# Kernel optimization log

Hardware: AMD Instinct MI355X
Metric: run time of the kernel (lower is better)

Reference implementation:

```python
import jax, jax.numpy as jnp
import numpy as np

B, S, D_IN, D_OUT = 4, 4096, 2048, 2048


def setup_inputs() -> dict:
    key = jax.random.key(0)
    kx, kw = jax.random.split(key)
    x = jax.random.normal(kx, (B, S, D_IN), dtype=jnp.float32)
    weight = jax.random.normal(kw, (D_OUT, D_IN), dtype=jnp.float32) * 0.02
    return {"x": x, "weight": weight}


def reference(x, weight):
    # Per-row absmax int8 activation quantization
    x_scale = jnp.clip(jnp.max(jnp.abs(x), axis=-1, keepdims=True), 1e-05, None)  # [B,S,1]
    x_quant = jnp.clip(jnp.round(x / x_scale * 127.0), -128.0, 127.0)
    # Ternary weight quantization (mean-centered absmean scale)
    w_mean = jnp.mean(weight)
    w_centered = weight - w_mean
    w_scale = jnp.clip(jnp.mean(jnp.abs(w_centered)), 1e-05, None)
    w_quant = jnp.clip(jnp.round(w_centered / w_scale), -1.0, 1.0)
    # GEMM on quantized values, then dequant rescale
    y = jnp.einsum('bsi,oi->bso', x_quant, w_quant)  # [B,S,D_OUT]
    y = y * (w_scale * x_scale / 127.0)
    return y.astype(x.dtype)
```

## Files before the change

kernel.cpp:

```cpp
#include <hip/hip_runtime.h>
#include <stdint.h>

#define M_TOT 16384
#define K_DIM 2048
#define N_DIM 2048
#define W_ELEMS (N_DIM * K_DIM)

typedef int v4i __attribute__((ext_vector_type(4)));

__device__ __forceinline__ void async_load16(const void* gptr, void* lptr) {
    __builtin_amdgcn_global_load_lds(
        (__attribute__((address_space(1))) void*)(uintptr_t)gptr,
        (__attribute__((address_space(3))) void*)(uint32_t)(uintptr_t)lptr,
        16, 0, 0);
}

__device__ __forceinline__ int qclamp(float v, int lo, int hi) {
    int q = (int)rintf(v);
    q = q > hi ? hi : (q < lo ? lo : q);
    return q & 255;
}

__global__ __launch_bounds__(256) void wsum_kernel(const float* __restrict__ w,
                                                   double* __restrict__ spart) {
    int tid = blockIdx.x * 256 + threadIdx.x;
    const float4* w4 = (const float4*)w;
    double s = 0.0;
    #pragma unroll
    for (int it = 0; it < 8; it++) {
        float4 v = w4[tid + it * 131072];
        s += (double)v.x + (double)v.y + (double)v.z + (double)v.w;
    }
    #pragma unroll
    for (int off = 32; off; off >>= 1) s += __shfl_down(s, off);
    __shared__ double ls[4];
    if ((threadIdx.x & 63) == 0) ls[threadIdx.x >> 6] = s;
    __syncthreads();
    if (threadIdx.x == 0) spart[blockIdx.x] = ls[0] + ls[1] + ls[2] + ls[3];
}

__global__ __launch_bounds__(256) void wabs_kernel(const float* __restrict__ w,
                                                   const double* __restrict__ spart,
                                                   double* __restrict__ apart) {
    __shared__ double ls[4];
    double sm = spart[threadIdx.x] + spart[threadIdx.x + 256];
    #pragma unroll
    for (int off = 32; off; off >>= 1) sm += __shfl_down(sm, off);
    if ((threadIdx.x & 63) == 0) ls[threadIdx.x >> 6] = sm;
    __syncthreads();
    double mean = (ls[0] + ls[1] + ls[2] + ls[3]) * (1.0 / (double)W_ELEMS);
    __syncthreads();
    int tid = blockIdx.x * 256 + threadIdx.x;
    const float4* w4 = (const float4*)w;
    double s = 0.0;
    #pragma unroll
    for (int it = 0; it < 8; it++) {
        float4 v = w4[tid + it * 131072];
        s += fabs((double)v.x - mean) + fabs((double)v.y - mean) +
             fabs((double)v.z - mean) + fabs((double)v.w - mean);
    }
    #pragma unroll
    for (int off = 32; off; off >>= 1) s += __shfl_down(s, off);
    if ((threadIdx.x & 63) == 0) ls[threadIdx.x >> 6] = s;
    __syncthreads();
    if (threadIdx.x == 0) apart[blockIdx.x] = ls[0] + ls[1] + ls[2] + ls[3];
}

__global__ __launch_bounds__(256) void quant_kernel(
    const float* __restrict__ x, const float* __restrict__ w,
    const double* __restrict__ spart, const double* __restrict__ apart,
    int8_t* __restrict__ xq, int8_t* __restrict__ wq,
    float* __restrict__ xscale, float* __restrict__ wsf)
{
    const int t = threadIdx.x;
    if (blockIdx.x < 4096) {
        const int row  = (blockIdx.x << 2) | (t >> 6);
        const int lane = t & 63;
        const float4* xr = (const float4*)(x + (size_t)row * K_DIM);
        float4 v[8];
        #pragma unroll
        for (int i = 0; i < 8; i++) v[i] = xr[lane + (i << 6)];
        float m = 0.0f;
        #pragma unroll
        for (int i = 0; i < 8; i++)
            m = fmaxf(m, fmaxf(fmaxf(fabsf(v[i].x), fabsf(v[i].y)),
                               fmaxf(fabsf(v[i].z), fabsf(v[i].w))));
        #pragma unroll
        for (int off = 32; off; off >>= 1) m = fmaxf(m, __shfl_xor(m, off));
        const float scale = fmaxf(m, 1e-5f);
        if (lane == 0) xscale[row] = scale;
        int* outp = (int*)(xq + (size_t)row * K_DIM);
        #pragma unroll
        for (int i = 0; i < 8; i++) {
            int p = qclamp(v[i].x / scale * 127.0f, -128, 127)
                  | (qclamp(v[i].y / scale * 127.0f, -128, 127) << 8)
                  | (qclamp(v[i].z / scale * 127.0f, -128, 127) << 16)
                  | (qclamp(v[i].w / scale * 127.0f, -128, 127) << 24);
            outp[lane + (i << 6)] = p;
        }
    } else {
        __shared__ double ls0[4], ls1[4];
        double s0 = spart[t] + spart[t + 256];
        double s1 = apart[t] + apart[t + 256];
        #pragma unroll
        for (int off = 32; off; off >>= 1) {
            s0 += __shfl_down(s0, off);
            s1 += __shfl_down(s1, off);
        }
        if ((t & 63) == 0) { ls0[t >> 6] = s0; ls1[t >> 6] = s1; }
        __syncthreads();
        float mean  = (float)((ls0[0] + ls0[1] + ls0[2] + ls0[3]) * (1.0 / (double)W_ELEMS));
        float scale = (float)fmax((ls1[0] + ls1[1] + ls1[2] + ls1[3]) * (1.0 / (double)W_ELEMS), 1e-5);
        int i = (blockIdx.x - 4096) * 256 + t;
        float4 v = ((const float4*)w)[i];
        int p = qclamp((v.x - mean) / scale, -1, 1)
              | (qclamp((v.y - mean) / scale, -1, 1) << 8)
              | (qclamp((v.z - mean) / scale, -1, 1) << 16)
              | (qclamp((v.w - mean) / scale, -1, 1) << 24);
        ((int*)wq)[i] = p;
        if (i == 0) wsf[0] = scale * (1.0f / 127.0f);
    }
}

__global__ __launch_bounds__(256, 2) void gemm_i8_kernel(
    const int8_t* __restrict__ xq, const int8_t* __restrict__ wq,
    const float* __restrict__ xscale, const float* __restrict__ wsf,
    float* __restrict__ out)
{
    __shared__ __align__(16) int8_t lsA[2][16384];
    __shared__ __align__(16) int8_t lsB[2][16384];

    const int tid  = threadIdx.x;
    const int lane = tid & 63;
    const int wv   = tid >> 6;

    const int flat = blockIdx.x;
    const int nf   = ((flat & 7) << 8) | (flat >> 3);
    const int bm   = nf >> 4;
    const int bn   = nf & 15;

    const int sChunk = ((tid & 3) ^ ((tid >> 3) & 3)) << 4;
    const int8_t* gAb = xq + (size_t)(bm * 128 + (tid >> 2)) * K_DIM + sChunk;
    const int8_t* gBb = wq + (size_t)(bn * 128 + (tid >> 2)) * K_DIM + sChunk;
    const int sDst = tid * 16;

    #define STAGE(OP, NB, K0, KH)                                              \
        do {                                                                   \
            async_load16(g##OP##b + (K0) + (KH) * 64,                          \
                         ls##OP[NB] + (KH) * 8192 + sDst);                     \
            async_load16(g##OP##b + (K0) + (KH) * 64 + (size_t)64 * K_DIM,     \
                         ls##OP[NB] + (KH) * 8192 + 4096 + sDst);              \
        } while (0)

    #define VM4 asm volatile("s_waitcnt vmcnt(4)" ::: "memory")
    #define VM0 asm volatile("s_waitcnt vmcnt(0)" ::: "memory")

    const int wm  = (wv >> 1) * 64;
    const int wn  = (wv & 1) * 64;
    const int fr  = lane & 15;
    const int fcl = lane >> 4;
    int aoff[4], boff[4];
    #pragma unroll
    for (int i = 0; i < 4; i++) {
        int ra = wm + i * 16 + fr;
        aoff[i] = ra * 64 + ((fcl ^ ((ra >> 1) & 3)) << 4);
        int rb = wn + i * 16 + fr;
        boff[i] = rb * 64 + ((fcl ^ ((rb >> 1) & 3)) << 4);
    }

    v4i acc[4][4] = {};

    #define PHASE(CB, KH, EXTRA)                                               \
        do {                                                                   \
            const int8_t* pA_ = lsA[CB] + (KH) * 8192;                         \
            const int8_t* pB_ = lsB[CB] + (KH) * 8192;                         \
            v4i af[4], bf[4];                                                  \
            _Pragma("unroll")                                                  \
            for (int i_ = 0; i_ < 4; i_++) {                                   \
                af[i_] = *(const v4i*)(pA_ + aoff[i_]);                        \
                bf[i_] = *(const v4i*)(pB_ + boff[i_]);                        \
            }                                                                  \
            EXTRA;                                                             \
            __builtin_amdgcn_s_barrier();                                      \
            __builtin_amdgcn_s_setprio(1);                                     \
            _Pragma("unroll")                                                  \
            for (int i_ = 0; i_ < 4; i_++)                                     \
                _Pragma("unroll")                                              \
                for (int j_ = 0; j_ < 4; j_++)                                 \
                    acc[i_][j_] = __builtin_amdgcn_mfma_i32_16x16x64_i8(       \
                        af[i_], bf[j_], acc[i_][j_], 0, 0, 0);                 \
            __builtin_amdgcn_s_setprio(0);                                     \
            __builtin_amdgcn_s_barrier();                                      \
        } while (0)

    STAGE(A, 0, 0, 0);
    STAGE(B, 0, 0, 0);
    STAGE(A, 0, 0, 1);
    STAGE(B, 0, 0, 1);
    VM4;
    __builtin_amdgcn_s_barrier();

    #pragma unroll 2
    for (int t = 0; t < 15; ++t) {
        const int cur = t & 1, nxt = cur ^ 1;
        const int kn = (t + 1) << 7;
        PHASE(cur, 0, STAGE(A, nxt, kn, 0); STAGE(B, nxt, kn, 0); VM4);
        PHASE(cur, 1, STAGE(A, nxt, kn, 1); STAGE(B, nxt, kn, 1); VM4);
    }
    PHASE(1, 0, (void)0);
    VM0;
    __builtin_amdgcn_s_barrier();
    PHASE(1, 1, (void)0);

    #undef PHASE
    #undef STAGE
    #undef VM4
    #undef VM0

    const float f127 = wsf[0];
    #pragma unroll
    for (int mi = 0; mi < 4; mi++) {
        #pragma unroll
        for (int rg = 0; rg < 4; rg++) {
            int mg = bm * 128 + wm + mi * 16 + (lane >> 4) * 4 + rg;
            float fs = f127 * xscale[mg];
            float* orow = out + (size_t)mg * N_DIM + bn * 128 + wn;
            #pragma unroll
            for (int nj = 0; nj < 4; nj++)
                orow[nj * 16 + fr] = fs * (float)acc[mi][nj][rg];
        }
    }
}

extern "C" void kernel_launch(void* const* d_in, const int* in_sizes, int n_in,
                              void* d_out, int out_size, void* d_ws, size_t ws_size,
                              hipStream_t stream) {
    const float* x = (const float*)d_in[0];
    const float* w = (const float*)d_in[1];
    float* out = (float*)d_out;

    char* ws = (char*)d_ws;
    double* spart  = (double*)ws;
    double* apart  = (double*)(ws + 4096);
    float*  wsf    = (float*)(ws + 8192);
    float*  xscale = (float*)(ws + 12288);
    int8_t* xq     = (int8_t*)(ws + 12288 + 65536);
    int8_t* wq     = xq + (size_t)M_TOT * K_DIM;

    wsum_kernel <<<512, 256, 0, stream>>>(w, spart);
    wabs_kernel <<<512, 256, 0, stream>>>(w, spart, apart);
    quant_kernel<<<8192, 256, 0, stream>>>(x, w, spart, apart, xq, wq, xscale, wsf);
    gemm_i8_kernel<<<2048, 256, 0, stream>>>(xq, wq, xscale, wsf, out);
}
```

Before: 318.1 us.

## Enlarge GEMM tile to 256x256 with 512 threads and 32x32x32 int8 MFMA

Reworks the int8 GEMM to use 256x256 output tiles per 512-thread block, 32x32x32 MFMA instructions, and full 128-wide K stages double-buffered in LDS. Larger tiles reduce global/L2 traffic for the quantized operands and the larger MFMA shape cuts LDS fragment reads per op. In exchange LDS use rises to 128KB per block, limiting occupancy, the pipeline is simplified to a full drain per iteration, and the grid shrinks to 512 blocks.

New measurement: 312.3 us. About the same (-1.8%).

```diff
diff --git a/kernel.cpp b/kernel.cpp
--- a/kernel.cpp
+++ b/kernel.cpp
@@ -6,7 +6,8 @@
 #define N_DIM 2048
 #define W_ELEMS (N_DIM * K_DIM)
 
-typedef int v4i __attribute__((ext_vector_type(4)));
+typedef int v4i  __attribute__((ext_vector_type(4)));
+typedef int v16i __attribute__((ext_vector_type(16)));
 
 __device__ __forceinline__ void async_load16(const void* gptr, void* lptr) {
     __builtin_amdgcn_global_load_lds(
@@ -122,112 +123,100 @@
     }
 }
 
-__global__ __launch_bounds__(256, 2) void gemm_i8_kernel(
+__global__ __launch_bounds__(512, 2) void gemm_i8_kernel(
     const int8_t* __restrict__ xq, const int8_t* __restrict__ wq,
     const float* __restrict__ xscale, const float* __restrict__ wsf,
     float* __restrict__ out)
 {
-    __shared__ __align__(16) int8_t lsA[2][16384];
-    __shared__ __align__(16) int8_t lsB[2][16384];
+    __shared__ __align__(16) int8_t lsA[2][32768];
+    __shared__ __align__(16) int8_t lsB[2][32768];
 
     const int tid  = threadIdx.x;
     const int lane = tid & 63;
     const int wv   = tid >> 6;
 
     const int flat = blockIdx.x;
-    const int nf   = ((flat & 7) << 8) | (flat >> 3);
-    const int bm   = nf >> 4;
-    const int bn   = nf & 15;
-
-    const int sChunk = ((tid & 3) ^ ((tid >> 3) & 3)) << 4;
-    const int8_t* gAb = xq + (size_t)(bm * 128 + (tid >> 2)) * K_DIM + sChunk;
-    const int8_t* gBb = wq + (size_t)(bn * 128 + (tid >> 2)) * K_DIM + sChunk;
+    const int nf   = ((flat & 7) << 6) | (flat >> 3);
+    const int bm   = nf >> 3;
+    const int bn   = nf & 7;
+
+    const int sChunk = (((tid & 7) ^ ((tid >> 3) & 7)) << 4);
+    const int8_t* gAb = xq + (size_t)(bm * 256 + (tid >> 3)) * K_DIM + sChunk;
+    const int8_t* gBb = wq + (size_t)(bn * 256 + (tid >> 3)) * K_DIM + sChunk;
     const int sDst = tid * 16;
 
-    #define STAGE(OP, NB, K0, KH)                                              \
+    #define STAGE(NB, K0)                                                      \
         do {                                                                   \
-            async_load16(g##OP##b + (K0) + (KH) * 64,                          \
-                         ls##OP[NB] + (KH) * 8192 + sDst);                     \
-            async_load16(g##OP##b + (K0) + (KH) * 64 + (size_t)64 * K_DIM,     \
-                         ls##OP[NB] + (KH) * 8192 + 4096 + sDst);              \
+            _Pragma("unroll")                                                  \
+            for (int g_ = 0; g_ < 4; g_++)                                     \
+                async_load16(gAb + (size_t)g_ * 64 * K_DIM + (K0),             \
+                             lsA[NB] + g_ * 8192 + sDst);                      \
+            _Pragma("unroll")                                                  \
+            for (int g_ = 0; g_ < 4; g_++)                                     \
+                async_load16(gBb + (size_t)g_ * 64 * K_DIM + (K0),             \
+                             lsB[NB] + g_ * 8192 + sDst);                      \
         } while (0)
 
-    #define VM4 asm volatile("s_waitcnt vmcnt(4)" ::: "memory")
-    #define VM0 asm volatile("s_waitcnt vmcnt(0)" ::: "memory")
-
-    const int wm  = (wv >> 1) * 64;
-    const int wn  = (wv & 1) * 64;
-    const int fr  = lane & 15;
-    const int fcl = lane >> 4;
-    int aoff[4], boff[4];
-    #pragma unroll
-    for (int i = 0; i < 4; i++) {
-        int ra = wm + i * 16 + fr;
-        aoff[i] = ra * 64 + ((fcl ^ ((ra >> 1) & 3)) << 4);
-        int rb = wn + i * 16 + fr;
-        boff[i] = rb * 64 + ((fcl ^ ((rb >> 1) & 3)) << 4);
-    }
-
-    v4i acc[4][4] = {};
-
-    #define PHASE(CB, KH, EXTRA)                                               \
-        do {                                                                   \
-            const int8_t* pA_ = lsA[CB] + (KH) * 8192;                         \
-            const int8_t* pB_ = lsB[CB] + (KH) * 8192;                         \
-            v4i af[4], bf[4];                                                  \
-            _Pragma("unroll")                                                  \
-            for (int i_ = 0; i_ < 4; i_++) {                                   \
-                af[i_] = *(const v4i*)(pA_ + aoff[i_]);                        \
-                bf[i_] = *(const v4i*)(pB_ + boff[i_]);                        \
-            }                                                                  \
-            EXTRA;                                                             \
-            __builtin_amdgcn_s_barrier();                                      \
-            __builtin_amdgcn_s_setprio(1);                                     \
-            _Pragma("unroll")                                                  \
-            for (int i_ = 0; i_ < 4; i_++)                                     \
-                _Pragma("unroll")                                              \
-                for (int j_ = 0; j_ < 4; j_++)                                 \
-                    acc[i_][j_] = __builtin_amdgcn_mfma_i32_16x16x64_i8(       \
-                        af[i_], bf[j_], acc[i_][j_], 0, 0, 0);                 \
-            __builtin_amdgcn_s_setprio(0);                                     \
-            __builtin_amdgcn_s_barrier();                                      \
-        } while (0)
-
-    STAGE(A, 0, 0, 0);
-    STAGE(B, 0, 0, 0);
-    STAGE(A, 0, 0, 1);
-    STAGE(B, 0, 0, 1);
-    VM4;
+    const int wm  = (wv >> 2) << 7;
+    const int wn  = (wv & 3) << 6;
+    const int l31 = lane & 31;
+    const int hi  = lane >> 5;
+    const int lx  = lane & 7;
+
+    int rA[4], rB[2], cs[4];
+    #pragma unroll
+    for (int mi = 0; mi < 4; mi++) rA[mi] = (wm + mi * 32 + l31) << 7;
+    #pragma unroll
+    for (int nj = 0; nj < 2; nj++) rB[nj] = (wn + nj * 32 + l31) << 7;
+    #pragma unroll
+    for (int ks = 0; ks < 4; ks++) cs[ks] = ((ks * 2 + hi) ^ lx) << 4;
+
+    v16i acc[4][2] = {};
+
+    STAGE(0, 0);
+    asm volatile("s_waitcnt vmcnt(0)" ::: "memory");
     __builtin_amdgcn_s_barrier();
 
-    #pragma unroll 2
-    for (int t = 0; t < 15; ++t) {
-        const int cur = t & 1, nxt = cur ^ 1;
-        const int kn = (t + 1) << 7;
-        PHASE(cur, 0, STAGE(A, nxt, kn, 0); STAGE(B, nxt, kn, 0); VM4);
-        PHASE(cur, 1, STAGE(A, nxt, kn, 1); STAGE(B, nxt, kn, 1); VM4);
-    }
-    PHASE(1, 0, (void)0);
-    VM0;
-    __builtin_amdgcn_s_barrier();
-    PHASE(1, 1, (void)0);
-
-    #undef PHASE
+    for (int t = 0; t < 16; ++t) {
+        const int cur = t & 1;
+        const int8_t* pA = lsA[cur];
+        const int8_t* pB = lsB[cur];
+        if (t < 15) STAGE(cur ^ 1, (t + 1) << 7);
+        __builtin_amdgcn_s_setprio(1);
+        #pragma unroll
+        for (int ks = 0; ks < 4; ks++) {
+            v4i af[4], bf[2];
+            #pragma unroll
+            for (int mi = 0; mi < 4; mi++)
+                af[mi] = *(const v4i*)(pA + rA[mi] + cs[ks]);
+            #pragma unroll
+            for (int nj = 0; nj < 2; nj++)
+                bf[nj] = *(const v4i*)(pB + rB[nj] + cs[ks]);
+            #pragma unroll
+            for (int mi = 0; mi < 4; mi++)
+                #pragma unroll
+                for (int nj = 0; nj < 2; nj++)
+                    acc[mi][nj] = __builtin_amdgcn_mfma_i32_32x32x32_i8(
+                        af[mi], bf[nj], acc[mi][nj], 0, 0, 0);
+        }
+        __builtin_amdgcn_s_setprio(0);
+        asm volatile("s_waitcnt vmcnt(0) lgkmcnt(0)" ::: "memory");
+        __builtin_amdgcn_s_barrier();
+    }
     #undef STAGE
-    #undef VM4
-    #undef VM0
 
     const float f127 = wsf[0];
     #pragma unroll
     for (int mi = 0; mi < 4; mi++) {
         #pragma unroll
-        for (int rg = 0; rg < 4; rg++) {
-            int mg = bm * 128 + wm + mi * 16 + (lane >> 4) * 4 + rg;
-            float fs = f127 * xscale[mg];
-            float* orow = out + (size_t)mg * N_DIM + bn * 128 + wn;
-            #pragma unroll
-            for (int nj = 0; nj < 4; nj++)
-                orow[nj * 16 + fr] = fs * (float)acc[mi][nj][rg];
+        for (int r = 0; r < 16; r++) {
+            const int rowl = (r & 3) + ((r >> 2) << 3) + (hi << 2);
+            const int mg = bm * 256 + wm + mi * 32 + rowl;
+            const float fs = f127 * xscale[mg];
+            float* orow = out + (size_t)mg * N_DIM + bn * 256 + wn + l31;
+            #pragma unroll
+            for (int nj = 0; nj < 2; nj++)
+                orow[nj * 32] = fs * (float)acc[mi][nj][r];
         }
     }
 }
@@ -250,5 +239,5 @@
     wsum_kernel <<<512, 256, 0, stream>>>(w, spart);
     wabs_kernel <<<512, 256, 0, stream>>>(w, spart, apart);
     quant_kernel<<<8192, 256, 0, stream>>>(x, w, spart, apart, xq, wq, xscale, wsf);
-    gemm_i8_kernel<<<2048, 256, 0, stream>>>(xq, wq, xscale, wsf, out);
-}
+    gemm_i8_kernel<<<512, 512, 0, stream>>>(xq, wq, xscale, wsf, out);
+}
```
